# Performance work log

Measured on AMD Instinct MI355X. Metric: run time of the kernel, lower is better.

The kernel has to match this reference:

```python
import jax, jax.numpy as jnp
import numpy as np

N = 512      # nodes
E = 16384    # edges (avg degree 32)
D = 128      # indim
OUT = 128    # outdim


def setup_inputs() -> dict:
    key = jax.random.key(0)
    k1, k2, k3 = jax.random.split(key, 3)
    X = jax.random.normal(k1, (N, N, D), dtype=jnp.float32)
    edge_index = jax.random.randint(k2, (2, E), 0, N, dtype=jnp.int64)
    W = jax.random.normal(k3, (3 * D, OUT), dtype=jnp.float32) * (1.0 / np.sqrt(3 * D))
    b = jnp.zeros((OUT,), dtype=jnp.float32)
    return {"X": X, "edge_index": edge_index, "W": W, "b": b}


def reference(X, edge_index, W, b):
    # X: [N, N, D] tuple features X[i, j] for (subgraph root i, node j)
    # edge_index: [2, E] directed edges (src -> dst), aggr = 'sum'
    n = X.shape[0]
    src, dst = edge_index[0], edge_index[1]
    # Dense binary adjacency (sum aggregation counts multi-edges, matching
    # scatter-add over the edge list). A[k, j] = #edges k -> j.
    A = jnp.zeros((n, n), dtype=X.dtype).at[src, dst].add(jnp.ones((src.shape[0],), X.dtype))
    # OpMessagePassingOnSubg2D: within subgraph i, aggregate over neighbors of j
    # X1[i, j] = sum_{k in N(j)} X[i, k]
    X1 = jnp.einsum('kj,ikd->ijd', A, X)
    # OpMessagePassingCrossSubg2D: across subgraphs, aggregate over neighbors of i
    # X2[i, j] = sum_{k in N(i)} X[k, j]
    X2 = jnp.einsum('ki,kjd->ijd', A, X)
    # catvalue([X1, X2]) -> [X, X1, X2], then pointwise MLP (single Linear)
    H = jnp.concatenate([X, X1, X2], axis=-1)  # [N, N, 3D]
    return H @ W + b  # [N, N, OUT]
```

## Files before the change

kernel.cpp:

```cpp
#include <hip/hip_runtime.h>
#include <hip/hip_bf16.h>
#include <stdint.h>

#define NN 512
#define DD 128
#define EE 16384

typedef short bf16x8 __attribute__((ext_vector_type(8)));
typedef short bf16x4 __attribute__((ext_vector_type(4)));
typedef float f32x4  __attribute__((ext_vector_type(4)));
typedef unsigned int u32;

__device__ __forceinline__ short f2bf(float f) {
    union { __hip_bfloat16 h; short s; } u;
    u.h = __float2bfloat16(f);
    return u.s;
}
__device__ __forceinline__ u32 pk2(float a, float b) {
    return (u32)(unsigned short)f2bf(a) | ((u32)(unsigned short)f2bf(b) << 16);
}

typedef __attribute__((address_space(3))) unsigned int lds_u32;
typedef __attribute__((address_space(1))) const unsigned int glb_u32;
__device__ __forceinline__ void gll16(void* l, const void* g) {
    __builtin_amdgcn_global_load_lds((glb_u32*)g, (lds_u32*)l, 16, 0, 0);
}


__global__ void k_zero(float* __restrict__ At) {
    At[blockIdx.x * 256 + threadIdx.x] = 0.0f;
}

__global__ void k_edges(const int* __restrict__ ei, float* __restrict__ At) {
    __shared__ int flag;
    if (threadIdx.x == 0) flag = 0;
    __syncthreads();
    int any = 0;
    for (int i = threadIdx.x; i < EE; i += blockDim.x) any |= ei[2 * i + 1];
    if (any) atomicOr(&flag, 1);
    __syncthreads();
    const bool is32 = (flag != 0);
    for (int e = threadIdx.x; e < EE; e += blockDim.x) {
        int src, dst;
        if (is32) { src = ei[e];     dst = ei[EE + e]; }
        else      { src = ei[2 * e]; dst = ei[2 * (EE + e)]; }
        atomicAdd(&At[dst * NN + src], 1.0f);
    }
}

__global__ void k_wt2(const float* __restrict__ W, short* __restrict__ Wt2) {
    int t = blockIdx.x * 256 + threadIdx.x;
    int kk = t >> 7, n = t & 127;
    int s = kk >> 7, d = kk & 127;
    Wt2[s * 16384 + n * 128 + d] = f2bf(W[t]);
}

__global__ void k_pack_at(const float* __restrict__ At, short* __restrict__ Atp) {
    int t = blockIdx.x * 256 + threadIdx.x;
    int T = t >> 6, l = t & 63;
    int row = (T >> 4) * 16 + (l & 15);
    int col = (T & 15) * 32 + (l >> 4) * 8;
    const float* s = &At[row * 512 + col];
    bf16x8 p;
    #pragma unroll
    for (int e = 0; e < 8; ++e) p[e] = f2bf(s[e]);
    *(bf16x8*)&Atp[(size_t)T * 512 + l * 8] = p;
}

__global__ __launch_bounds__(256) void k_y(const float* __restrict__ X,
                                           const short* __restrict__ Wt2,
                                           short* __restrict__ Y1T,
                                           short* __restrict__ Y2) {
    __shared__ __align__(16) short Xs[16384];
    __shared__ __align__(16) short Ws[16384];

    const int tid  = threadIdx.x;
    const int lane = tid & 63;
    const int wv   = tid >> 6;
    const int wr   = (wv >> 1) * 64;
    const int wc   = (wv & 1) * 64;
    const int lm   = lane & 15;
    const int lq   = lane >> 4;
    const int i  = blockIdx.x >> 2;
    const int j0 = (blockIdx.x & 3) * 128;

    #pragma unroll
    for (int it = 0; it < 16; ++it) {
        int g = tid + it * 256;
        int r = g >> 5, c4 = g & 31;
        float4 v = *(const float4*)&X[i * 65536 + (j0 + r) * 128 + c4 * 4];
        int kb = c4 >> 4, c = c4 & 15, p = c >> 1, h2 = c & 1;
        bf16x4 pc; pc[0] = f2bf(v.x); pc[1] = f2bf(v.y); pc[2] = f2bf(v.z); pc[3] = f2bf(v.w);
        *(bf16x4*)&Xs[kb * 8192 + r * 64 + ((p ^ (r & 7)) * 8 + h2 * 4)] = pc;
    }

    #pragma unroll
    for (int s = 1; s <= 2; ++s) {
        #pragma unroll
        for (int it = 0; it < 8; ++it) {
            int slot = it * 256 + tid;
            int kb = slot >> 10, rem = slot & 1023;
            int n = rem >> 3, pc = rem & 7;
            gll16(&Ws[slot * 8],
                  &Wt2[s * 16384 + n * 128 + kb * 64 + ((pc ^ (n & 7)) * 8)]);
        }
        __syncthreads();

        f32x4 acc[4][4] = {};
        #pragma unroll
        for (int kb = 0; kb < 2; ++kb)
            #pragma unroll
            for (int ks = 0; ks < 2; ++ks) {
                bf16x8 af[4], bf[4];
                #pragma unroll
                for (int mf = 0; mf < 4; ++mf) {
                    int R = wr + mf * 16 + lm, Cc = ks * 4 + lq;
                    af[mf] = *(const bf16x8*)&Xs[kb * 8192 + R * 64 + (Cc ^ (R & 7)) * 8];
                }
                #pragma unroll
                for (int nf = 0; nf < 4; ++nf) {
                    int R = wc + nf * 16 + lm, Cc = ks * 4 + lq;
                    bf[nf] = *(const bf16x8*)&Ws[kb * 8192 + R * 64 + (Cc ^ (R & 7)) * 8];
                }
                #pragma unroll
                for (int mf = 0; mf < 4; ++mf)
                    #pragma unroll
                    for (int nf = 0; nf < 4; ++nf)
                        acc[mf][nf] = __builtin_amdgcn_mfma_f32_16x16x32_bf16(
                            af[mf], bf[nf], acc[mf][nf], 0, 0, 0);
            }
        __syncthreads();

        if (s == 1) {
            u32* T = (u32*)Ws;
            #pragma unroll
            for (int mf = 0; mf < 4; ++mf)
                #pragma unroll
                for (int nf = 0; nf < 4; ++nf) {
                    int n = wc + nf * 16 + lm;
                    int jb = wr + mf * 16 + lq * 4;
                    int w = jb >> 1;
                    u32 lo = pk2(acc[mf][nf][0], acc[mf][nf][1]);
                    u32 hi = pk2(acc[mf][nf][2], acc[mf][nf][3]);
                    uint2 val; val.x = lo; val.y = hi;
                    *(uint2*)&T[n * 64 + (w ^ (n & 28))] = val;
                }
            __syncthreads();
            #pragma unroll
            for (int it = 0; it < 8; ++it) {
                int ch = tid & 15, n = (tid >> 4) + it * 16;
                uint4 q = *(const uint4*)&T[n * 64 + ((ch * 4) ^ (n & 28))];
                *(uint4*)&Y1T[i * 65536 + n * 512 + j0 + ch * 8] = q;
            }
            __syncthreads();
        } else {
            #pragma unroll
            for (int mf = 0; mf < 4; ++mf)
                #pragma unroll
                for (int nf = 0; nf < 4; ++nf)
                    #pragma unroll
                    for (int r = 0; r < 4; ++r)
                        Ws[(wr + mf * 16 + lq * 4 + r) * 128 + wc + nf * 16 + lm]
                            = f2bf(acc[mf][nf][r]);
            __syncthreads();
            #pragma unroll
            for (int it = 0; it < 8; ++it) {
                int q = tid + it * 256;
                int row = q >> 4, oc = (q & 15) * 8;
                *(bf16x8*)&Y2[i * 65536 + (j0 + row) * 128 + oc]
                    = *(const bf16x8*)&Ws[row * 128 + oc];
            }
        }
    }
}

__global__ __launch_bounds__(256) void k_t(const short* __restrict__ Y2,
                                           short* __restrict__ Y2T) {
    __shared__ __align__(16) u32 U[128 * 64];
    const int tid = threadIdx.x;
    const int bid = (blockIdx.x & 7) * 256 + (blockIdx.x >> 3);
    const int j  = bid >> 2;
    const int k0 = (bid & 3) * 128;

    const int c8 = tid & 15;
    const int a0 = tid >> 4;
    #pragma unroll
    for (int it = 0; it < 4; ++it) {
        int a = a0 + it * 16;
        const short* r0 = &Y2[(size_t)(k0 + 2 * a) * 65536 + j * 128 + c8 * 8];
        bf16x8 A0 = *(const bf16x8*)r0;
        bf16x8 A1 = *(const bf16x8*)(r0 + 65536);
        #pragma unroll
        for (int cc = 0; cc < 8; ++cc) {
            int n = c8 * 8 + cc;
            U[n * 64 + (a ^ (n & 28))] =
                (u32)(unsigned short)A0[cc] | ((u32)(unsigned short)A1[cc] << 16);
        }
    }
    __syncthreads();
    const int ch = tid & 15;
    const int n0 = tid >> 4;
    #pragma unroll
    for (int it = 0; it < 8; ++it) {
        int n = n0 + it * 16;
        uint4 q = *(const uint4*)&U[n * 64 + ((ch * 4) ^ (n & 28))];
        *(uint4*)&Y2T[j * 65536 + n * 512 + k0 + ch * 8] = q;
    }
}

__global__ __launch_bounds__(256) void k_a1(const short* __restrict__ Atp,
                                            const short* __restrict__ Y1T,
                                            short* __restrict__ P1) {
    __shared__ __align__(16) short sm[16384];

    const int tid  = threadIdx.x;
    const int lane = tid & 63;
    const int wv   = tid >> 6;
    const int wr   = (wv >> 1) * 64;
    const int wc   = (wv & 1) * 64;
    const int lm   = lane & 15;
    const int lq   = lane >> 4;
    const int bid = (blockIdx.x & 7) * 256 + (blockIdx.x >> 3);
    const int i  = bid >> 2;
    const int a0 = (bid & 3) * 128;
    const int jt0 = (a0 >> 4) + (wr >> 4);

    f32x4 acc[4][4] = {};

    #pragma unroll
    for (int it = 0; it < 4; ++it) {
        int slot = it * 256 + tid;
        int r = slot >> 3, p = slot & 7;
        int cg = (p ^ (r & 7)) * 8;
        gll16(&sm[slot * 8], &Y1T[i * 65536 + r * 512 + cg]);
    }
    __syncthreads();

    for (int kb = 0; kb < 8; ++kb) {
        short* cur = (kb & 1) ? sm + 8192 : sm;
        short* nxt = (kb & 1) ? sm : sm + 8192;

        bf16x8 afr[2][4];
        #pragma unroll
        for (int ks = 0; ks < 2; ++ks)
            #pragma unroll
            for (int mf = 0; mf < 4; ++mf)
                afr[ks][mf] = *(const bf16x8*)&Atp[(size_t)((jt0 + mf) * 16 + kb * 2 + ks) * 512 + lane * 8];
        __builtin_amdgcn_sched_barrier(0);

        if (kb < 7) {
            const int k0n = (kb + 1) * 64;
            #pragma unroll
            for (int it = 0; it < 4; ++it) {
                int slot = it * 256 + tid;
                int r = slot >> 3, p = slot & 7;
                int cg = (p ^ (r & 7)) * 8;
                gll16(&nxt[slot * 8], &Y1T[i * 65536 + r * 512 + k0n + cg]);
            }
        }

        #pragma unroll
        for (int ks = 0; ks < 2; ++ks) {
            bf16x8 bf[4];
            #pragma unroll
            for (int nf = 0; nf < 4; ++nf) {
                int R = wc + nf * 16 + lm, Cc = ks * 4 + lq;
                bf[nf] = *(const bf16x8*)&cur[R * 64 + (Cc ^ (R & 7)) * 8];
            }
            #pragma unroll
            for (int mf = 0; mf < 4; ++mf)
                #pragma unroll
                for (int nf = 0; nf < 4; ++nf)
                    acc[mf][nf] = __builtin_amdgcn_mfma_f32_16x16x32_bf16(
                        afr[ks][mf], bf[nf], acc[mf][nf], 0, 0, 0);
        }
        __syncthreads();
    }

    #pragma unroll
    for (int mf = 0; mf < 4; ++mf)
        #pragma unroll
        for (int nf = 0; nf < 4; ++nf)
            #pragma unroll
            for (int r = 0; r < 4; ++r)
                sm[(wr + mf * 16 + lq * 4 + r) * 128 + wc + nf * 16 + lm]
                    = f2bf(acc[mf][nf][r]);
    __syncthreads();
    #pragma unroll
    for (int it = 0; it < 8; ++it) {
        int q = tid + it * 256;
        int row = q >> 4, oc = (q & 15) * 8;
        *(bf16x8*)&P1[i * 65536 + (a0 + row) * 128 + oc]
            = *(const bf16x8*)&sm[row * 128 + oc];
    }
}

__global__ __launch_bounds__(256) void k_a2f(const float* __restrict__ X,
                                             const short* __restrict__ Atp,
                                             const short* __restrict__ Y2T,
                                             const short* __restrict__ Wt2,
                                             const short* __restrict__ P1,
                                             const float* __restrict__ bias,
                                             float* __restrict__ out) {
    __shared__ __align__(16) short sm[16384];
    short* As = sm;
    short* Bs = sm + 8192;

    const int tid  = threadIdx.x;
    const int lane = tid & 63;
    const int wv   = tid >> 6;
    const int wr   = (wv >> 1) * 64;
    const int wc   = (wv & 1) * 64;
    const int lm   = lane & 15;
    const int lq   = lane >> 4;
    const int bid = (blockIdx.x & 7) * 256 + (blockIdx.x >> 3);
    const int j  = bid >> 2;
    const int i0 = (bid & 3) * 128;

    f32x4 acc[4][4] = {};

    #pragma unroll
    for (int kb = 0; kb < 2; ++kb) {
        #pragma unroll
        for (int it = 0; it < 8; ++it) {
            int g = tid + it * 256;
            int r = g >> 4, c4 = g & 15;
            float4 v = *(const float4*)&X[(size_t)(i0 + r) * 65536 + j * 128 + kb * 64 + c4 * 4];
            int p = c4 >> 1, h2 = c4 & 1;
            bf16x4 pc; pc[0] = f2bf(v.x); pc[1] = f2bf(v.y); pc[2] = f2bf(v.z); pc[3] = f2bf(v.w);
            *(bf16x4*)&As[r * 64 + ((p ^ (r & 7)) * 8 + h2 * 4)] = pc;
        }
        #pragma unroll
        for (int it = 0; it < 4; ++it) {
            int slot = it * 256 + tid;
            int n = slot >> 3, pc = slot & 7;
            gll16(&Bs[slot * 8], &Wt2[n * 128 + kb * 64 + ((pc ^ (n & 7)) * 8)]);
        }
        __syncthreads();
        #pragma unroll
        for (int ks = 0; ks < 2; ++ks) {
            bf16x8 af[4], bf[4];
            #pragma unroll
            for (int mf = 0; mf < 4; ++mf) {
                int R = wr + mf * 16 + lm, Cc = ks * 4 + lq;
                af[mf] = *(const bf16x8*)&As[R * 64 + (Cc ^ (R & 7)) * 8];
            }
            #pragma unroll
            for (int nf = 0; nf < 4; ++nf) {
                int R = wc + nf * 16 + lm, Cc = ks * 4 + lq;
                bf[nf] = *(const bf16x8*)&Bs[R * 64 + (Cc ^ (R & 7)) * 8];
            }
            #pragma unroll
            for (int mf = 0; mf < 4; ++mf)
                #pragma unroll
                for (int nf = 0; nf < 4; ++nf)
                    acc[mf][nf] = __builtin_amdgcn_mfma_f32_16x16x32_bf16(
                        af[mf], bf[nf], acc[mf][nf], 0, 0, 0);
        }
        __syncthreads();
    }

    const int jt0 = (i0 >> 4) + (wr >> 4);
    #pragma unroll
    for (int it = 0; it < 4; ++it) {
        int slot = it * 256 + tid;
        int r = slot >> 3, p = slot & 7;
        int cg = (p ^ (r & 7)) * 8;
        gll16(&sm[slot * 8], &Y2T[j * 65536 + r * 512 + cg]);
    }
    __syncthreads();

    for (int kb = 0; kb < 8; ++kb) {
        short* cur = (kb & 1) ? sm + 8192 : sm;
        short* nxt = (kb & 1) ? sm : sm + 8192;

        bf16x8 afr[2][4];
        #pragma unroll
        for (int ks = 0; ks < 2; ++ks)
            #pragma unroll
            for (int mf = 0; mf < 4; ++mf)
                afr[ks][mf] = *(const bf16x8*)&Atp[(size_t)((jt0 + mf) * 16 + kb * 2 + ks) * 512 + lane * 8];
        __builtin_amdgcn_sched_barrier(0);

        if (kb < 7) {
            const int k0n = (kb + 1) * 64;
            #pragma unroll
            for (int it = 0; it < 4; ++it) {
                int slot = it * 256 + tid;
                int r = slot >> 3, p = slot & 7;
                int cg = (p ^ (r & 7)) * 8;
                gll16(&nxt[slot * 8], &Y2T[j * 65536 + r * 512 + k0n + cg]);
            }
        }

        #pragma unroll
        for (int ks = 0; ks < 2; ++ks) {
            bf16x8 bf[4];
            #pragma unroll
            for (int nf = 0; nf < 4; ++nf) {
                int R = wc + nf * 16 + lm, Cc = ks * 4 + lq;
                bf[nf] = *(const bf16x8*)&cur[R * 64 + (Cc ^ (R & 7)) * 8];
            }
            #pragma unroll
            for (int mf = 0; mf < 4; ++mf)
                #pragma unroll
                for (int nf = 0; nf < 4; ++nf)
                    acc[mf][nf] = __builtin_amdgcn_mfma_f32_16x16x32_bf16(
                        afr[ks][mf], bf[nf], acc[mf][nf], 0, 0, 0);
        }
        __syncthreads();
    }

    #pragma unroll
    for (int mf = 0; mf < 4; ++mf)
        #pragma unroll
        for (int nf = 0; nf < 4; ++nf)
            #pragma unroll
            for (int r = 0; r < 4; ++r)
                sm[(wr + mf * 16 + lq * 4 + r) * 128 + wc + nf * 16 + lm]
                    = f2bf(acc[mf][nf][r]);
    __syncthreads();
    #pragma unroll
    for (int it = 0; it < 8; ++it) {
        int q = tid + it * 256;
        int row = q >> 4, oc = (q & 15) * 8;
        bf16x8 vs = *(const bf16x8*)&sm[row * 128 + oc];
        bf16x8 vpl = *(const bf16x8*)&P1[(size_t)(i0 + row) * 65536 + j * 128 + oc];
        float4 b0 = *(const float4*)&bias[oc];
        float4 b1 = *(const float4*)&bias[oc + 4];
        union { short s; __hip_bfloat16 h; } cs, cp;
        float o[8];
        #pragma unroll
        for (int e = 0; e < 8; ++e) {
            cs.s = vs[e]; cp.s = vpl[e];
            o[e] = __bfloat162float(cs.h) + __bfloat162float(cp.h);
        }
        o[0] += b0.x; o[1] += b0.y; o[2] += b0.z; o[3] += b0.w;
        o[4] += b1.x; o[5] += b1.y; o[6] += b1.z; o[7] += b1.w;
        float* op = &out[(size_t)(i0 + row) * 65536 + j * 128 + oc];
        float4 w0; w0.x = o[0]; w0.y = o[1]; w0.z = o[2]; w0.w = o[3];
        float4 w1; w1.x = o[4]; w1.y = o[5]; w1.z = o[6]; w1.w = o[7];
        *(float4*)op = w0;
        *(float4*)(op + 4) = w1;
    }
}


__global__ __launch_bounds__(256) void k_agg_fb(const float* __restrict__ X,
                                                const float* __restrict__ At,
                                                short* __restrict__ X1b,
                                                short* __restrict__ X2b) {
    __shared__ short As[128 * 72];
    __shared__ short Bs[128 * 72];
    const int tid  = threadIdx.x;
    const int lane = tid & 63;
    const int wv   = tid >> 6;
    const int wr   = (wv >> 1) * 64;
    const int wc   = (wv & 1) * 64;
    const int lm   = lane & 15;
    const int lq   = lane >> 4;
    int a0, Bbase, Bks, Cbase, Crs;
    short* Cp;
    const int bidx = blockIdx.x;
    if (bidx < 2048) {
        int i = bidx >> 2, jt = bidx & 3;
        a0 = jt * 128; Bbase = i * 65536; Bks = 128;
        Cbase = i * 65536 + jt * 16384; Crs = 128; Cp = X1b;
    } else {
        int bb = bidx - 2048;
        int j = bb >> 2, it = bb & 3;
        a0 = it * 128; Bbase = j * 128; Bks = 65536;
        Cbase = it * 8388608 + j * 128; Crs = 65536; Cp = X2b;
    }
    f32x4 acc[4][4] = {};
    const int d  = tid & 127;
    const int kh = tid >> 7;
    for (int kb = 0; kb < 8; ++kb) {
        const int k0 = kb * 64;
        #pragma unroll
        for (int it8 = 0; it8 < 8; ++it8) {
            int g = tid + it8 * 256;
            int r = g >> 4, kq = (g & 15) * 4;
            float4 v = *(const float4*)&At[(a0 + r) * 512 + k0 + kq];
            bf16x4 p; p[0] = f2bf(v.x); p[1] = f2bf(v.y); p[2] = f2bf(v.z); p[3] = f2bf(v.w);
            *(bf16x4*)&As[r * 72 + kq] = p;
        }
        #pragma unroll
        for (int gi = 0; gi < 4; ++gi) {
            int kg = kh * 4 + gi;
            bf16x8 p;
            #pragma unroll
            for (int jj = 0; jj < 8; ++jj)
                p[jj] = f2bf(X[Bbase + (k0 + kg * 8 + jj) * Bks + d]);
            *(bf16x8*)&Bs[d * 72 + kg * 8] = p;
        }
        __syncthreads();
        #pragma unroll
        for (int ks = 0; ks < 2; ++ks) {
            bf16x8 af[4], bfr[4];
            #pragma unroll
            for (int mf = 0; mf < 4; ++mf)
                af[mf] = *(const bf16x8*)&As[(wr + mf * 16 + lm) * 72 + ks * 32 + lq * 8];
            #pragma unroll
            for (int nf = 0; nf < 4; ++nf)
                bfr[nf] = *(const bf16x8*)&Bs[(wc + nf * 16 + lm) * 72 + ks * 32 + lq * 8];
            #pragma unroll
            for (int mf = 0; mf < 4; ++mf)
                #pragma unroll
                for (int nf = 0; nf < 4; ++nf)
                    acc[mf][nf] = __builtin_amdgcn_mfma_f32_16x16x32_bf16(
                        af[mf], bfr[nf], acc[mf][nf], 0, 0, 0);
        }
        __syncthreads();
    }
    #pragma unroll
    for (int mf = 0; mf < 4; ++mf)
        #pragma unroll
        for (int nf = 0; nf < 4; ++nf)
            #pragma unroll
            for (int r = 0; r < 4; ++r) {
                int row = wr + mf * 16 + lq * 4 + r;
                int col = wc + nf * 16 + lm;
                Cp[Cbase + row * Crs + col] = f2bf(acc[mf][nf][r]);
            }
}

__global__ __launch_bounds__(256) void k_final_fb(const float* __restrict__ X,
                                                  const short* __restrict__ X1b,
                                                  const short* __restrict__ X2b,
                                                  const short* __restrict__ Wt2,
                                                  const float* __restrict__ bias,
                                                  float* __restrict__ out) {
    __shared__ short As[128 * 72];
    __shared__ short Ws[128 * 72];
    const int tid  = threadIdx.x;
    const int lane = tid & 63;
    const int wv   = tid >> 6;
    const int wr   = (wv >> 1) * 64;
    const int wc   = (wv & 1) * 64;
    const int lm   = lane & 15;
    const int lq   = lane >> 4;
    const int m0   = blockIdx.x * 128;
    f32x4 acc[4][4] = {};
    for (int ph = 0; ph < 6; ++ph) {
        const int s = ph >> 1, h = ph & 1;
        if (s == 0) {
            #pragma unroll
            for (int it8 = 0; it8 < 8; ++it8) {
                int g = tid + it8 * 256;
                int r = g >> 4, kq = (g & 15) * 4;
                float4 v = *(const float4*)&X[(m0 + r) * 128 + h * 64 + kq];
                bf16x4 p; p[0] = f2bf(v.x); p[1] = f2bf(v.y); p[2] = f2bf(v.z); p[3] = f2bf(v.w);
                *(bf16x4*)&As[r * 72 + kq] = p;
            }
        } else {
            const short* src = (s == 1) ? X1b : X2b;
            #pragma unroll
            for (int it4 = 0; it4 < 4; ++it4) {
                int g = tid + it4 * 256;
                int r = g >> 3, ko = (g & 7) * 8;
                *(bf16x8*)&As[r * 72 + ko] =
                    *(const bf16x8*)&src[(m0 + r) * 128 + h * 64 + ko];
            }
        }
        #pragma unroll
        for (int it4 = 0; it4 < 4; ++it4) {
            int g = tid + it4 * 256;
            int n = g >> 3, ko = (g & 7) * 8;
            *(bf16x8*)&Ws[n * 72 + ko] =
                *(const bf16x8*)&Wt2[s * 16384 + n * 128 + h * 64 + ko];
        }
        __syncthreads();
        #pragma unroll
        for (int ks = 0; ks < 2; ++ks) {
            bf16x8 af[4], bfr[4];
            #pragma unroll
            for (int mf = 0; mf < 4; ++mf)
                af[mf] = *(const bf16x8*)&As[(wr + mf * 16 + lm) * 72 + ks * 32 + lq * 8];
            #pragma unroll
            for (int nf = 0; nf < 4; ++nf)
                bfr[nf] = *(const bf16x8*)&Ws[(wc + nf * 16 + lm) * 72 + ks * 32 + lq * 8];
            #pragma unroll
            for (int mf = 0; mf < 4; ++mf)
                #pragma unroll
                for (int nf = 0; nf < 4; ++nf)
                    acc[mf][nf] = __builtin_amdgcn_mfma_f32_16x16x32_bf16(
                        af[mf], bfr[nf], acc[mf][nf], 0, 0, 0);
        }
        __syncthreads();
    }
    #pragma unroll
    for (int nf = 0; nf < 4; ++nf) {
        float bv = bias[wc + nf * 16 + lm];
        #pragma unroll
        for (int mf = 0; mf < 4; ++mf)
            #pragma unroll
            for (int r = 0; r < 4; ++r) {
                int row = m0 + wr + mf * 16 + lq * 4 + r;
                int col = wc + nf * 16 + lm;
                out[row * 128 + col] = acc[mf][nf][r] + bv;
            }
    }
}

extern "C" void kernel_launch(void* const* d_in, const int* in_sizes, int n_in,
                              void* d_out, int out_size, void* d_ws, size_t ws_size,
                              hipStream_t stream) {
    const float* X  = (const float*)d_in[0];
    const int*   ei = (const int*)d_in[1];
    const float* W  = (const float*)d_in[2];
    const float* b  = (const float*)d_in[3];
    float* out = (float*)d_out;
    char* ws = (char*)d_ws;
    const size_t MB = 1u << 20;

    float* At  = (float*)ws;
    short* Atp = (short*)(ws + 1 * MB);
    short* Wt2 = (short*)(ws + 1 * MB + 512 * 1024);

    k_zero   <<<1024, 256, 0, stream>>>(At);
    k_edges  <<<1, 1024, 0, stream>>>(ei, At);
    k_wt2    <<<192, 256, 0, stream>>>(W, Wt2);
    k_pack_at<<<128, 256, 0, stream>>>(At, Atp);

    if (ws_size >= 194 * MB) {
        short* Y1T = (short*)(ws + 2 * MB);
        short* Y2  = (short*)(ws + 66 * MB);
        short* Y2T = (short*)(ws + 130 * MB);
        short* P1  = Y2;
        k_y  <<<2048, 256, 0, stream>>>(X, Wt2, Y1T, Y2);
        k_t  <<<2048, 256, 0, stream>>>(Y2, Y2T);
        k_a1 <<<2048, 256, 0, stream>>>(Atp, Y1T, P1);
        k_a2f<<<2048, 256, 0, stream>>>(X, Atp, Y2T, Wt2, P1, b, out);
    } else {
        short* X1b = (short*)(ws + 2 * MB);
        short* X2b = (short*)(ws + 66 * MB);
        k_agg_fb  <<<4096, 256, 0, stream>>>(X, At, X1b, X2b);
        k_final_fb<<<2048, 256, 0, stream>>>(X, X1b, X2b, Wt2, b, out);
    }
}
```

Before: 487.5 us.

## Widen aggregation GEMM tiles to 128x256 with 512-thread blocks and pre-packed W0

Replaces k_a1 and k_a2f with k_p1 and k_f, which flatten the (subgraph, node) axes into a combined N dimension and compute 128x256 output tiles using 8 waves per block. Each A-fragment load from Atp is then reused across twice as many columns, and the X·W0 term reads its B operand directly from a new MFMA-fragment-packed W0 buffer instead of staging it through LDS. The intermediate P1 layout changes to match the new tiling. This costs more LDS per block (64 KB), more waves per block, and an extra small packing kernel.

After: 675.5 us. 38.6% more time.

```diff
diff --git a/kernel.cpp b/kernel.cpp
--- a/kernel.cpp
+++ b/kernel.cpp
@@ -65,6 +65,18 @@
     #pragma unroll
     for (int e = 0; e < 8; ++e) p[e] = f2bf(s[e]);
     *(bf16x8*)&Atp[(size_t)T * 512 + l * 8] = p;
+}
+
+__global__ void k_pack_w0(const float* __restrict__ W, short* __restrict__ W0p) {
+    int t = blockIdx.x * 256 + threadIdx.x;
+    int T = t >> 6, l = t & 63;
+    int nt = T >> 2, kt = T & 3;
+    int n  = nt * 16 + (l & 15);
+    int d0 = kt * 32 + (l >> 4) * 8;
+    bf16x8 p;
+    #pragma unroll
+    for (int e = 0; e < 8; ++e) p[e] = f2bf(W[(d0 + e) * 128 + n]);
+    *(bf16x8*)&W0p[(size_t)T * 512 + l * 8] = p;
 }
 
 __global__ __launch_bounds__(256) void k_y(const float* __restrict__ X,
@@ -208,37 +220,36 @@
     }
 }
 
-__global__ __launch_bounds__(256) void k_a1(const short* __restrict__ Atp,
-                                            const short* __restrict__ Y1T,
-                                            short* __restrict__ P1) {
-    __shared__ __align__(16) short sm[16384];
+__global__ __launch_bounds__(512, 4) void k_p1(const short* __restrict__ Atp,
+                                               const short* __restrict__ Y1T,
+                                               short* __restrict__ P1x) {
+    __shared__ __align__(16) short sm[32768];
 
     const int tid  = threadIdx.x;
     const int lane = tid & 63;
     const int wv   = tid >> 6;
-    const int wr   = (wv >> 1) * 64;
-    const int wc   = (wv & 1) * 64;
+    const int wrM  = (wv >> 2) * 64;
+    const int wcN  = (wv & 3) * 64;
     const int lm   = lane & 15;
     const int lq   = lane >> 4;
-    const int bid = (blockIdx.x & 7) * 256 + (blockIdx.x >> 3);
-    const int i  = bid >> 2;
-    const int a0 = (bid & 3) * 128;
-    const int jt0 = (a0 >> 4) + (wr >> 4);
+    const int lin = (blockIdx.x & 7) * 128 + (blockIdx.x >> 3);
+    const int j0 = (lin & 3) * 128;
+    const int N0 = (lin >> 2) * 256;
+    const int jt0 = (j0 >> 4) + (wrM >> 4);
 
     f32x4 acc[4][4] = {};
 
     #pragma unroll
     for (int it = 0; it < 4; ++it) {
-        int slot = it * 256 + tid;
+        int slot = it * 512 + tid;
         int r = slot >> 3, p = slot & 7;
-        int cg = (p ^ (r & 7)) * 8;
-        gll16(&sm[slot * 8], &Y1T[i * 65536 + r * 512 + cg]);
+        gll16(&sm[slot * 8], &Y1T[(size_t)(N0 + r) * 512 + ((p ^ (r & 7)) * 8)]);
     }
     __syncthreads();
 
     for (int kb = 0; kb < 8; ++kb) {
-        short* cur = (kb & 1) ? sm + 8192 : sm;
-        short* nxt = (kb & 1) ? sm : sm + 8192;
+        short* cur = (kb & 1) ? sm + 16384 : sm;
+        short* nxt = (kb & 1) ? sm : sm + 16384;
 
         bf16x8 afr[2][4];
         #pragma unroll
@@ -252,10 +263,9 @@
             const int k0n = (kb + 1) * 64;
             #pragma unroll
             for (int it = 0; it < 4; ++it) {
-                int slot = it * 256 + tid;
+                int slot = it * 512 + tid;
                 int r = slot >> 3, p = slot & 7;
-                int cg = (p ^ (r & 7)) * 8;
-                gll16(&nxt[slot * 8], &Y1T[i * 65536 + r * 512 + k0n + cg]);
+                gll16(&nxt[slot * 8], &Y1T[(size_t)(N0 + r) * 512 + k0n + ((p ^ (r & 7)) * 8)]);
             }
         }
 
@@ -264,7 +274,7 @@
             bf16x8 bf[4];
             #pragma unroll
             for (int nf = 0; nf < 4; ++nf) {
-                int R = wc + nf * 16 + lm, Cc = ks * 4 + lq;
+                int R = wcN + nf * 16 + lm, Cc = ks * 4 + lq;
                 bf[nf] = *(const bf16x8*)&cur[R * 64 + (Cc ^ (R & 7)) * 8];
             }
             #pragma unroll
@@ -282,114 +292,108 @@
         #pragma unroll
         for (int nf = 0; nf < 4; ++nf)
             #pragma unroll
-            for (int r = 0; r < 4; ++r)
-                sm[(wr + mf * 16 + lq * 4 + r) * 128 + wc + nf * 16 + lm]
-                    = f2bf(acc[mf][nf][r]);
+            for (int rr = 0; rr < 4; ++rr)
+                sm[(wrM + mf * 16 + lq * 4 + rr) * 256 + wcN + nf * 16 + lm]
+                    = f2bf(acc[mf][nf][rr]);
     __syncthreads();
     #pragma unroll
     for (int it = 0; it < 8; ++it) {
-        int q = tid + it * 256;
-        int row = q >> 4, oc = (q & 15) * 8;
-        *(bf16x8*)&P1[i * 65536 + (a0 + row) * 128 + oc]
-            = *(const bf16x8*)&sm[row * 128 + oc];
-    }
-}
-
-__global__ __launch_bounds__(256) void k_a2f(const float* __restrict__ X,
-                                             const short* __restrict__ Atp,
-                                             const short* __restrict__ Y2T,
-                                             const short* __restrict__ Wt2,
-                                             const short* __restrict__ P1,
-                                             const float* __restrict__ bias,
-                                             float* __restrict__ out) {
-    __shared__ __align__(16) short sm[16384];
-    short* As = sm;
-    short* Bs = sm + 8192;
+        int q = tid + it * 512;
+        int row = q >> 5, oc = (q & 31) * 8;
+        *(bf16x8*)&P1x[(size_t)(j0 + row) * 65536 + N0 + oc]
+            = *(const bf16x8*)&sm[row * 256 + oc];
+    }
+}
+
+__global__ __launch_bounds__(512, 4) void k_f(const float* __restrict__ X,
+                                              const short* __restrict__ Atp,
+                                              const short* __restrict__ Y2T,
+                                              const short* __restrict__ W0p,
+                                              const short* __restrict__ P1x,
+                                              const float* __restrict__ bias,
+                                              float* __restrict__ out) {
+    __shared__ __align__(16) short sm[32768];
 
     const int tid  = threadIdx.x;
     const int lane = tid & 63;
     const int wv   = tid >> 6;
-    const int wr   = (wv >> 1) * 64;
-    const int wc   = (wv & 1) * 64;
+    const int wrM  = (wv >> 2) * 64;
+    const int wcN  = (wv & 3) * 64;
     const int lm   = lane & 15;
     const int lq   = lane >> 4;
-    const int bid = (blockIdx.x & 7) * 256 + (blockIdx.x >> 3);
-    const int j  = bid >> 2;
-    const int i0 = (bid & 3) * 128;
+    const int lin = (blockIdx.x & 7) * 128 + (blockIdx.x >> 3);
+    const int i0  = (lin & 3) * 128;
+    const int N0  = (lin >> 2) * 256;
+    const int jb0 = N0 >> 7;
 
     f32x4 acc[4][4] = {};
 
     #pragma unroll
-    for (int kb = 0; kb < 2; ++kb) {
-        #pragma unroll
-        for (int it = 0; it < 8; ++it) {
-            int g = tid + it * 256;
-            int r = g >> 4, c4 = g & 15;
-            float4 v = *(const float4*)&X[(size_t)(i0 + r) * 65536 + j * 128 + kb * 64 + c4 * 4];
-            int p = c4 >> 1, h2 = c4 & 1;
-            bf16x4 pc; pc[0] = f2bf(v.x); pc[1] = f2bf(v.y); pc[2] = f2bf(v.z); pc[3] = f2bf(v.w);
-            *(bf16x4*)&As[r * 64 + ((p ^ (r & 7)) * 8 + h2 * 4)] = pc;
-        }
-        #pragma unroll
-        for (int it = 0; it < 4; ++it) {
-            int slot = it * 256 + tid;
-            int n = slot >> 3, pc = slot & 7;
-            gll16(&Bs[slot * 8], &Wt2[n * 128 + kb * 64 + ((pc ^ (n & 7)) * 8)]);
-        }
-        __syncthreads();
-        #pragma unroll
-        for (int ks = 0; ks < 2; ++ks) {
-            bf16x8 af[4], bf[4];
-            #pragma unroll
-            for (int mf = 0; mf < 4; ++mf) {
-                int R = wr + mf * 16 + lm, Cc = ks * 4 + lq;
-                af[mf] = *(const bf16x8*)&As[R * 64 + (Cc ^ (R & 7)) * 8];
-            }
-            #pragma unroll
-            for (int nf = 0; nf < 4; ++nf) {
-                int R = wc + nf * 16 + lm, Cc = ks * 4 + lq;
-                bf[nf] = *(const bf16x8*)&Bs[R * 64 + (Cc ^ (R & 7)) * 8];
-            }
-            #pragma unroll
-            for (int mf = 0; mf < 4; ++mf)
+    for (int it = 0; it < 16; ++it) {
+        int g = tid + it * 512;
+        int r = g >> 6, c4 = g & 63;
+        float4 v = *(const float4*)&X[(size_t)(i0 + r) * 65536 + jb0 * 128 + c4 * 4];
+        int jp = c4 >> 5, cc = c4 & 31;
+        int kb = cc >> 4, c = cc & 15, p = c >> 1, h2 = c & 1;
+        bf16x4 pc; pc[0] = f2bf(v.x); pc[1] = f2bf(v.y); pc[2] = f2bf(v.z); pc[3] = f2bf(v.w);
+        *(bf16x4*)&sm[jp * 16384 + kb * 8192 + r * 64 + ((p ^ (r & 7)) * 8 + h2 * 4)] = pc;
+    }
+    __syncthreads();
+    {
+        const int jpw = (wv & 3) >> 1;
+        const int ntb = (wv & 1) * 4;
+        #pragma unroll
+        for (int kb = 0; kb < 2; ++kb)
+            #pragma unroll
+            for (int ks = 0; ks < 2; ++ks) {
+                int kt = kb * 2 + ks, Cc = ks * 4 + lq;
+                bf16x8 af[4], bf[4];
+                #pragma unroll
+                for (int mf = 0; mf < 4; ++mf) {
+                    int R = wrM + mf * 16 + lm;
+                    af[mf] = *(const bf16x8*)&sm[jpw * 16384 + kb * 8192 + R * 64 + ((Cc ^ (R & 7)) * 8)];
+                }
                 #pragma unroll
                 for (int nf = 0; nf < 4; ++nf)
-                    acc[mf][nf] = __builtin_amdgcn_mfma_f32_16x16x32_bf16(
-                        af[mf], bf[nf], acc[mf][nf], 0, 0, 0);
-        }
-        __syncthreads();
-    }
-
-    const int jt0 = (i0 >> 4) + (wr >> 4);
+                    bf[nf] = *(const bf16x8*)&W0p[(size_t)((ntb + nf) * 4 + kt) * 512 + lane * 8];
+                #pragma unroll
+                for (int mf = 0; mf < 4; ++mf)
+                    #pragma unroll
+                    for (int nf = 0; nf < 4; ++nf)
+                        acc[mf][nf] = __builtin_amdgcn_mfma_f32_16x16x32_bf16(
+                            af[mf], bf[nf], acc[mf][nf], 0, 0, 0);
+            }
+    }
+    __syncthreads();
+
+    const int it0 = (i0 >> 4) + (wrM >> 4);
     #pragma unroll
     for (int it = 0; it < 4; ++it) {
-        int slot = it * 256 + tid;
+        int slot = it * 512 + tid;
         int r = slot >> 3, p = slot & 7;
-        int cg = (p ^ (r & 7)) * 8;
-        gll16(&sm[slot * 8], &Y2T[j * 65536 + r * 512 + cg]);
+        gll16(&sm[slot * 8], &Y2T[(size_t)(N0 + r) * 512 + ((p ^ (r & 7)) * 8)]);
     }
     __syncthreads();
 
     for (int kb = 0; kb < 8; ++kb) {
-        short* cur = (kb & 1) ? sm + 8192 : sm;
-        short* nxt = (kb & 1) ? sm : sm + 8192;
+        short* cur = (kb & 1) ? sm + 16384 : sm;
+        short* nxt = (kb & 1) ? sm : sm + 16384;
 
         bf16x8 afr[2][4];
         #pragma unroll
         for (int ks = 0; ks < 2; ++ks)
             #pragma unroll
             for (int mf = 0; mf < 4; ++mf)
-                afr[ks][mf] = *(const bf16x8*)&Atp[(size_t)((jt0 + mf) * 16 + kb * 2 + ks) * 512 + lane * 8];
+                afr[ks][mf] = *(const bf16x8*)&Atp[(size_t)((it0 + mf) * 16 + kb * 2 + ks) * 512 + lane * 8];
         __builtin_amdgcn_sched_barrier(0);
 
         if (kb < 7) {
             const int k0n = (kb + 1) * 64;
             #pragma unroll
             for (int it = 0; it < 4; ++it) {
-                int slot = it * 256 + tid;
+                int slot = it * 512 + tid;
                 int r = slot >> 3, p = slot & 7;
-                int cg = (p ^ (r & 7)) * 8;
-                gll16(&nxt[slot * 8], &Y2T[j * 65536 + r * 512 + k0n + cg]);
+                gll16(&nxt[slot * 8], &Y2T[(size_t)(N0 + r) * 512 + k0n + ((p ^ (r & 7)) * 8)]);
             }
         }
 
@@ -398,7 +402,7 @@
             bf16x8 bf[4];
             #pragma unroll
             for (int nf = 0; nf < 4; ++nf) {
-                int R = wc + nf * 16 + lm, Cc = ks * 4 + lq;
+                int R = wcN + nf * 16 + lm, Cc = ks * 4 + lq;
                 bf[nf] = *(const bf16x8*)&cur[R * 64 + (Cc ^ (R & 7)) * 8];
             }
             #pragma unroll
@@ -416,18 +420,19 @@
         #pragma unroll
         for (int nf = 0; nf < 4; ++nf)
             #pragma unroll
-            for (int r = 0; r < 4; ++r)
-                sm[(wr + mf * 16 + lq * 4 + r) * 128 + wc + nf * 16 + lm]
-                    = f2bf(acc[mf][nf][r]);
+            for (int rr = 0; rr < 4; ++rr)
+                sm[(wrM + mf * 16 + lq * 4 + rr) * 256 + wcN + nf * 16 + lm]
+                    = f2bf(acc[mf][nf][rr]);
     __syncthreads();
     #pragma unroll
     for (int it = 0; it < 8; ++it) {
-        int q = tid + it * 256;
-        int row = q >> 4, oc = (q & 15) * 8;
-        bf16x8 vs = *(const bf16x8*)&sm[row * 128 + oc];
-        bf16x8 vpl = *(const bf16x8*)&P1[(size_t)(i0 + row) * 65536 + j * 128 + oc];
-        float4 b0 = *(const float4*)&bias[oc];
-        float4 b1 = *(const float4*)&bias[oc + 4];
+        int q = tid + it * 512;
+        int row = q >> 5, oc = (q & 31) * 8;
+        int jp2 = oc >> 7, n = oc & 127;
+        bf16x8 vs = *(const bf16x8*)&sm[row * 256 + oc];
+        bf16x8 vpl = *(const bf16x8*)&P1x[(size_t)(jb0 + jp2) * 65536 + (i0 + row) * 128 + n];
+        float4 b0 = *(const float4*)&bias[n];
+        float4 b1 = *(const float4*)&bias[n + 4];
         union { short s; __hip_bfloat16 h; } cs, cp;
         float o[8];
         #pragma unroll
@@ -437,7 +442,7 @@
         }
         o[0] += b0.x; o[1] += b0.y; o[2] += b0.z; o[3] += b0.w;
         o[4] += b1.x; o[5] += b1.y; o[6] += b1.z; o[7] += b1.w;
-        float* op = &out[(size_t)(i0 + row) * 65536 + j * 128 + oc];
+        float* op = &out[(size_t)(i0 + row) * 65536 + N0 + oc];
         float4 w0; w0.x = o[0]; w0.y = o[1]; w0.z = o[2]; w0.w = o[3];
         float4 w1; w1.x = o[4]; w1.y = o[5]; w1.z = o[6]; w1.w = o[7];
         *(float4*)op = w0;
@@ -617,21 +622,23 @@
     float* At  = (float*)ws;
     short* Atp = (short*)(ws + 1 * MB);
     short* Wt2 = (short*)(ws + 1 * MB + 512 * 1024);
+    short* W0p = (short*)(ws + 1 * MB + 608 * 1024);
 
     k_zero   <<<1024, 256, 0, stream>>>(At);
     k_edges  <<<1, 1024, 0, stream>>>(ei, At);
     k_wt2    <<<192, 256, 0, stream>>>(W, Wt2);
     k_pack_at<<<128, 256, 0, stream>>>(At, Atp);
+    k_pack_w0<<<8, 256, 0, stream>>>(W, W0p);
 
     if (ws_size >= 194 * MB) {
         short* Y1T = (short*)(ws + 2 * MB);
         short* Y2  = (short*)(ws + 66 * MB);
         short* Y2T = (short*)(ws + 130 * MB);
-        short* P1  = Y2;
-        k_y  <<<2048, 256, 0, stream>>>(X, Wt2, Y1T, Y2);
-        k_t  <<<2048, 256, 0, stream>>>(Y2, Y2T);
-        k_a1 <<<2048, 256, 0, stream>>>(Atp, Y1T, P1);
-        k_a2f<<<2048, 256, 0, stream>>>(X, Atp, Y2T, Wt2, P1, b, out);
+        short* P1x = Y2;
+        k_y <<<2048, 256, 0, stream>>>(X, Wt2, Y1T, Y2);
+        k_t <<<2048, 256, 0, stream>>>(Y2, Y2T);
+        k_p1<<<1024, 512, 0, stream>>>(Atp, Y1T, P1x);
+        k_f <<<1024, 512, 0, stream>>>(X, Atp, Y2T, W0p, P1x, b, out);
     } else {
         short* X1b = (short*)(ws + 2 * MB);
         short* X2b = (short*)(ws + 66 * MB);
```
